# Kernel tuning notes

Measured on AMD Instinct MI355X. Metric: run time of the kernel, lower is better.

The kernel has to match this reference:

```python
import jax, jax.numpy as jnp
import numpy as np

B, S, D, H = 4, 2048, 768, 12
HD = D // H  # head_dim = 64
NEG = 1e10
EPS = 1e-5

def setup_inputs() -> dict:
    key = jax.random.key(0)
    k1, k2, k3 = jax.random.split(key, 3)
    return {
        "context": jax.random.normal(k1, (B, S, D), dtype=jnp.float32),
        "pad_mask": jnp.ones((B, S), dtype=jnp.float32),
        "w_qkv": jax.random.normal(k2, (D, 3 * D), dtype=jnp.float32) * 0.02,
        "w_proj": jax.random.normal(k3, (D, D), dtype=jnp.float32) * (0.02 / np.sqrt(2.0 * 12)),
        "b_proj": jnp.zeros((D,), dtype=jnp.float32),
        "gamma": jnp.ones((D,), dtype=jnp.float32),
        "beta": jnp.zeros((D,), dtype=jnp.float32),
    }

def reference(context, pad_mask, w_qkv, w_proj, b_proj, gamma, beta):
    b, s, d = context.shape
    resid = context
    qkv = context @ w_qkv                       # [B,S,3D]
    q, k, v = jnp.split(qkv, 3, axis=-1)
    # [B,S,D] -> [B,H,S,HD]
    q = q.reshape(b, s, H, HD).transpose(0, 2, 1, 3)
    k = k.reshape(b, s, H, HD).transpose(0, 2, 1, 3)
    v = v.reshape(b, s, H, HD).transpose(0, 2, 1, 3)
    scores = jnp.einsum("bhqd,bhkd->bhqk", q, k) * (1.0 / np.sqrt(HD))
    m = pad_mask[:, None, None, :]              # [B,1,1,S]
    scores = scores * m - (1.0 - m) * NEG       # multiplicative mask + big negative
    attn = jax.nn.softmax(scores, axis=-1)      # dropout is identity at inference
    out = jnp.einsum("bhqk,bhkd->bhqd", attn, v)
    out = out.transpose(0, 2, 1, 3).reshape(b, s, d)
    out = out @ w_proj + b_proj
    x = out + resid
    mu = jnp.mean(x, axis=-1, keepdims=True)
    var = jnp.var(x, axis=-1, keepdims=True)
    return (x - mu) * jax.lax.rsqrt(var + EPS) * gamma + beta
```

## Files before the change

kernel.cpp:

```cpp
#include <hip/hip_runtime.h>

#define BB 4
#define SS 2048
#define DD 768
#define HH 12
#define HDD 64
#define BS (BB*SS)
#define NQKV (3*DD)
#define NEL (BS*DD)

typedef __attribute__((ext_vector_type(8))) __bf16 bf16x8;
typedef __attribute__((ext_vector_type(4))) float fx4;
typedef __attribute__((ext_vector_type(4))) int   ix4;

#define MFMA16(a,b,c) __builtin_amdgcn_mfma_f32_16x16x32_bf16((a),(b),(c),0,0,0)

__device__ __forceinline__ unsigned short f2bf(float f) {
  unsigned u = __builtin_bit_cast(unsigned, f);
  u = (u + 0x7FFFu + ((u >> 16) & 1u)) >> 16;
  return (unsigned short)u;
}
__device__ __forceinline__ unsigned pkbf(float a, float b) {
  unsigned ua = __builtin_bit_cast(unsigned, a);
  unsigned ub = __builtin_bit_cast(unsigned, b);
  return ((ua + 0x8000u) >> 16) | ((ub + 0x8000u) & 0xFFFF0000u);
}

__global__ __launch_bounds__(256) void pack_bf16(const float* __restrict__ x,
                                                 unsigned short* __restrict__ y, int n4) {
  int i = blockIdx.x * 256 + threadIdx.x;
  if (i < n4) {
    float4 v = ((const float4*)x)[i];
    ((uint2*)y)[i] = make_uint2(pkbf(v.x, v.y), pkbf(v.z, v.w));
  }
}

__global__ __launch_bounds__(256) void pack_transpose(const float* __restrict__ w,
                                                      unsigned short* __restrict__ wT,
                                                      int K, int N) {
  __shared__ unsigned short t[32][33];
  int n0 = blockIdx.x * 32, k0 = blockIdx.y * 32;
  int tx = threadIdx.x & 31, ty = threadIdx.x >> 5;
#pragma unroll
  for (int r = ty; r < 32; r += 8)
    t[tx][r] = f2bf(w[(size_t)(k0 + r) * N + n0 + tx]);
  __syncthreads();
#pragma unroll
  for (int r = ty; r < 32; r += 8)
    wT[(size_t)(n0 + r) * K + k0 + tx] = t[r][tx];
}

__global__ __launch_bounds__(256) void gemm_qkv_k(const unsigned short* __restrict__ Wt,
                                                  const unsigned short* __restrict__ X,
                                                  unsigned short* __restrict__ Qo,
                                                  unsigned short* __restrict__ Ko,
                                                  unsigned short* __restrict__ Vto) {
  __shared__ unsigned short As[128 * 32];
  __shared__ unsigned short Bs[128 * 32];
  const int tid = threadIdx.x;
  const int w = tid >> 6, lane = tid & 63, quad = lane >> 4, l16 = lane & 15;
  const int m0 = blockIdx.y << 7;
  const int n0 = blockIdx.x << 7;
  const int wm = (w & 1) * 64, wn = (w >> 1) * 64;
  fx4 acc[4][4];
#pragma unroll
  for (int i = 0; i < 4; ++i)
#pragma unroll
    for (int c = 0; c < 4; ++c) acc[i][c] = (fx4){0.f, 0.f, 0.f, 0.f};

  const int c0 = tid, c1 = 256 + tid;
  const unsigned short* Ag0 = Wt + (size_t)(m0 + (c0 >> 2)) * DD + (c0 & 3) * 8;
  const unsigned short* Ag1 = Wt + (size_t)(m0 + (c1 >> 2)) * DD + (c1 & 3) * 8;
  const unsigned short* Bg0 = X + (size_t)(n0 + (c0 >> 2)) * DD + (c0 & 3) * 8;
  const unsigned short* Bg1 = X + (size_t)(n0 + (c1 >> 2)) * DD + (c1 & 3) * 8;

  ix4 ra0 = *(const ix4*)Ag0;
  ix4 ra1 = *(const ix4*)Ag1;
  ix4 rb0 = *(const ix4*)Bg0;
  ix4 rb1 = *(const ix4*)Bg1;

  for (int k0 = 0; k0 < DD; k0 += 32) {
    __syncthreads();
    *(ix4*)((char*)As + c0 * 16) = ra0;
    *(ix4*)((char*)As + c1 * 16) = ra1;
    *(ix4*)((char*)Bs + c0 * 16) = rb0;
    *(ix4*)((char*)Bs + c1 * 16) = rb1;
    __syncthreads();
    if (k0 + 32 < DD) {
      ra0 = *(const ix4*)(Ag0 + k0 + 32);
      ra1 = *(const ix4*)(Ag1 + k0 + 32);
      rb0 = *(const ix4*)(Bg0 + k0 + 32);
      rb1 = *(const ix4*)(Bg1 + k0 + 32);
    }
    bf16x8 af[4], bf[4];
#pragma unroll
    for (int i = 0; i < 4; ++i) af[i] = *(const bf16x8*)&As[(wm + i * 16 + l16) * 32 + quad * 8];
#pragma unroll
    for (int c = 0; c < 4; ++c) bf[c] = *(const bf16x8*)&Bs[(wn + c * 16 + l16) * 32 + quad * 8];
#pragma unroll
    for (int i = 0; i < 4; ++i)
#pragma unroll
      for (int c = 0; c < 4; ++c) acc[i][c] = MFMA16(af[i], bf[c], acc[i][c]);
  }

  const int which = m0 / DD;
#pragma unroll
  for (int i = 0; i < 4; ++i) {
    int fb = m0 + wm + i * 16 + quad * 4;
    int d = fb - which * DD;
    int h = d >> 6, hd = d & 63;
#pragma unroll
    for (int c = 0; c < 4; ++c) {
      int srow = n0 + wn + c * 16 + l16;
      int b = srow >> 11, s = srow & (SS - 1);
      if (which == 0) {
        uint2 v = make_uint2(pkbf(acc[i][c][0], acc[i][c][1]), pkbf(acc[i][c][2], acc[i][c][3]));
        *(uint2*)&Qo[((size_t)(b * HH + h) * SS + s) * HDD + hd] = v;
      } else if (which == 1) {
        uint2 v = make_uint2(pkbf(acc[i][c][0], acc[i][c][1]), pkbf(acc[i][c][2], acc[i][c][3]));
        *(uint2*)&Ko[((size_t)(b * HH + h) * SS + s) * HDD + hd] = v;
      } else {
#pragma unroll
        for (int r = 0; r < 4; ++r)
          Vto[((size_t)(b * HH + h) * HDD + hd + r) * SS + s] = f2bf(acc[i][c][r]);
      }
    }
  }
}

__global__ __launch_bounds__(256) void gemm_proj_k(const unsigned short* __restrict__ Wt,
                                                   const unsigned short* __restrict__ X,
                                                   const float* __restrict__ ctx,
                                                   const float* __restrict__ bproj,
                                                   float* __restrict__ xf) {
  __shared__ unsigned short As[128 * 32];
  __shared__ unsigned short Bs[128 * 32];
  const int tid = threadIdx.x;
  const int w = tid >> 6, lane = tid & 63, quad = lane >> 4, l16 = lane & 15;
  const int m0 = blockIdx.y << 7;
  const int n0 = blockIdx.x << 7;
  const int wm = (w & 1) * 64, wn = (w >> 1) * 64;
  fx4 acc[4][4];
#pragma unroll
  for (int i = 0; i < 4; ++i)
#pragma unroll
    for (int c = 0; c < 4; ++c) acc[i][c] = (fx4){0.f, 0.f, 0.f, 0.f};

  const int c0 = tid, c1 = 256 + tid;
  const unsigned short* Ag0 = Wt + (size_t)(m0 + (c0 >> 2)) * DD + (c0 & 3) * 8;
  const unsigned short* Ag1 = Wt + (size_t)(m0 + (c1 >> 2)) * DD + (c1 & 3) * 8;
  const unsigned short* Bg0 = X + (size_t)(n0 + (c0 >> 2)) * DD + (c0 & 3) * 8;
  const unsigned short* Bg1 = X + (size_t)(n0 + (c1 >> 2)) * DD + (c1 & 3) * 8;

  ix4 ra0 = *(const ix4*)Ag0;
  ix4 ra1 = *(const ix4*)Ag1;
  ix4 rb0 = *(const ix4*)Bg0;
  ix4 rb1 = *(const ix4*)Bg1;

  for (int k0 = 0; k0 < DD; k0 += 32) {
    __syncthreads();
    *(ix4*)((char*)As + c0 * 16) = ra0;
    *(ix4*)((char*)As + c1 * 16) = ra1;
    *(ix4*)((char*)Bs + c0 * 16) = rb0;
    *(ix4*)((char*)Bs + c1 * 16) = rb1;
    __syncthreads();
    if (k0 + 32 < DD) {
      ra0 = *(const ix4*)(Ag0 + k0 + 32);
      ra1 = *(const ix4*)(Ag1 + k0 + 32);
      rb0 = *(const ix4*)(Bg0 + k0 + 32);
      rb1 = *(const ix4*)(Bg1 + k0 + 32);
    }
    bf16x8 af[4], bf[4];
#pragma unroll
    for (int i = 0; i < 4; ++i) af[i] = *(const bf16x8*)&As[(wm + i * 16 + l16) * 32 + quad * 8];
#pragma unroll
    for (int c = 0; c < 4; ++c) bf[c] = *(const bf16x8*)&Bs[(wn + c * 16 + l16) * 32 + quad * 8];
#pragma unroll
    for (int i = 0; i < 4; ++i)
#pragma unroll
      for (int c = 0; c < 4; ++c) acc[i][c] = MFMA16(af[i], bf[c], acc[i][c]);
  }

#pragma unroll
  for (int i = 0; i < 4; ++i) {
    int fb = m0 + wm + i * 16 + quad * 4;
    float4 bp = *(const float4*)&bproj[fb];
#pragma unroll
    for (int c = 0; c < 4; ++c) {
      int srow = n0 + wn + c * 16 + l16;
      float4 cx = *(const float4*)&ctx[(size_t)srow * DD + fb];
      float4 r;
      r.x = acc[i][c][0] + bp.x + cx.x;
      r.y = acc[i][c][1] + bp.y + cx.y;
      r.z = acc[i][c][2] + bp.z + cx.z;
      r.w = acc[i][c][3] + bp.w + cx.w;
      *(float4*)&xf[(size_t)srow * DD + fb] = r;
    }
  }
}

__global__ __launch_bounds__(256) void attn_k(const unsigned short* __restrict__ Q,
                                              const unsigned short* __restrict__ K,
                                              const unsigned short* __restrict__ Vt,
                                              const float* __restrict__ mask,
                                              unsigned short* __restrict__ O) {
  __shared__ unsigned short Ks[64 * 64];
  __shared__ unsigned short Vts[64 * 64];
  const int tid = threadIdx.x;
  const int w = tid >> 6, lane = tid & 63;
  const int quad = lane >> 4, l16 = lane & 15;
  const int bh = blockIdx.y;
  const int b = bh / HH, h = bh - b * HH;
  const int q0 = blockIdx.x << 7;
  const unsigned short* Qb = Q + (size_t)bh * (SS * HDD);
  const unsigned short* Kb = K + (size_t)bh * (SS * HDD);
  const unsigned short* Vtb = Vt + (size_t)bh * (SS * HDD);
  const float* mb = mask + b * SS;

  bf16x8 qf[2][2];
#pragma unroll
  for (int qi = 0; qi < 2; ++qi)
#pragma unroll
    for (int f = 0; f < 2; ++f)
      qf[qi][f] = *(const bf16x8*)&Qb[(size_t)(q0 + w * 32 + qi * 16 + l16) * HDD + f * 32 + quad * 8];

  fx4 o[2][4];
#pragma unroll
  for (int qi = 0; qi < 2; ++qi)
#pragma unroll
    for (int ht = 0; ht < 4; ++ht) o[qi][ht] = (fx4){0.f, 0.f, 0.f, 0.f};
  float lsum[2] = {0.f, 0.f};

  const int cA = tid, cB = 256 + tid;
  const int rA = cA >> 3, pA = (cA & 7) ^ (rA & 7);
  const int rB = cB >> 3, pB = (cB & 7) ^ (rB & 7);

  ix4 rk0 = *(const ix4*)&Kb[(size_t)rA * HDD + pA * 8];
  ix4 rk1 = *(const ix4*)&Kb[(size_t)rB * HDD + pB * 8];
  ix4 rv0 = *(const ix4*)&Vtb[(size_t)rA * SS + pA * 8];
  ix4 rv1 = *(const ix4*)&Vtb[(size_t)rB * SS + pB * 8];

  for (int k0 = 0; k0 < SS; k0 += 64) {
    __syncthreads();
    *(ix4*)((char*)Ks + cA * 16) = rk0;
    *(ix4*)((char*)Ks + cB * 16) = rk1;
    *(ix4*)((char*)Vts + cA * 16) = rv0;
    *(ix4*)((char*)Vts + cB * 16) = rv1;
    __syncthreads();
    if (k0 + 64 < SS) {
      int kn = k0 + 64;
      rk0 = *(const ix4*)&Kb[(size_t)(kn + rA) * HDD + pA * 8];
      rk1 = *(const ix4*)&Kb[(size_t)(kn + rB) * HDD + pB * 8];
      rv0 = *(const ix4*)&Vtb[(size_t)rA * SS + kn + pA * 8];
      rv1 = *(const ix4*)&Vtb[(size_t)rB * SS + kn + pB * 8];
    }

    float4 mq[4];
#pragma unroll
    for (int kt = 0; kt < 4; ++kt)
      mq[kt] = *(const float4*)&mb[k0 + kt * 16 + quad * 4];

    bf16x8 kf[4][2];
#pragma unroll
    for (int kt = 0; kt < 4; ++kt) {
      int row = kt * 16 + l16;
      int rx = row & 7;
#pragma unroll
      for (int f = 0; f < 2; ++f)
        kf[kt][f] = *(const bf16x8*)&Ks[row * 64 + ((f * 4 + quad) ^ rx) * 8];
    }
    bf16x8 vf[4][2];
#pragma unroll
    for (int ht = 0; ht < 4; ++ht) {
      int row = ht * 16 + l16;
      int rx = row & 7;
#pragma unroll
      for (int f = 0; f < 2; ++f) {
        int dc0 = (f * 4 + (quad >> 1)) ^ rx;
        int dc1 = (f * 4 + 2 + (quad >> 1)) ^ rx;
        uint2 lo = *(const uint2*)((const char*)Vts + row * 128 + dc0 * 16 + (quad & 1) * 8);
        uint2 hi = *(const uint2*)((const char*)Vts + row * 128 + dc1 * 16 + (quad & 1) * 8);
        ix4 vv = (ix4){(int)lo.x, (int)lo.y, (int)hi.x, (int)hi.y};
        vf[ht][f] = __builtin_bit_cast(bf16x8, vv);
      }
    }

#pragma unroll
    for (int qi = 0; qi < 2; ++qi) {
      fx4 sc[4];
#pragma unroll
      for (int kt = 0; kt < 4; ++kt) {
        fx4 s = (fx4){0.f, 0.f, 0.f, 0.f};
        s = MFMA16(kf[kt][0], qf[qi][0], s);
        s = MFMA16(kf[kt][1], qf[qi][1], s);
        sc[kt] = s;
      }
      unsigned pk[4][2];
      float ls = 0.f;
#pragma unroll
      for (int kt = 0; kt < 4; ++kt) {
        float p[4];
#pragma unroll
        for (int r = 0; r < 4; ++r) {
          float mv = ((const float*)&mq[kt])[r];
          p[r] = __expf(sc[kt][r] * (0.125f * mv) - (1.f - mv) * 1e10f);
          ls += p[r];
        }
        pk[kt][0] = pkbf(p[0], p[1]);
        pk[kt][1] = pkbf(p[2], p[3]);
      }
      lsum[qi] += ls;
      ix4 p0 = (ix4){(int)pk[0][0], (int)pk[0][1], (int)pk[1][0], (int)pk[1][1]};
      ix4 p1 = (ix4){(int)pk[2][0], (int)pk[2][1], (int)pk[3][0], (int)pk[3][1]};
      bf16x8 pf0 = __builtin_bit_cast(bf16x8, p0);
      bf16x8 pf1 = __builtin_bit_cast(bf16x8, p1);
#pragma unroll
      for (int ht = 0; ht < 4; ++ht) {
        o[qi][ht] = MFMA16(vf[ht][0], pf0, o[qi][ht]);
        o[qi][ht] = MFMA16(vf[ht][1], pf1, o[qi][ht]);
      }
    }
  }

#pragma unroll
  for (int qi = 0; qi < 2; ++qi) {
    float t = lsum[qi];
    t += __shfl_xor(t, 16);
    t += __shfl_xor(t, 32);
    float inv = 1.f / fmaxf(t, 1e-30f);
    int sq = q0 + w * 32 + qi * 16 + l16;
    unsigned short* orow = O + ((size_t)(b * SS + sq)) * DD + h * HDD;
#pragma unroll
    for (int ht = 0; ht < 4; ++ht) {
      uint2 v = make_uint2(pkbf(o[qi][ht][0] * inv, o[qi][ht][1] * inv),
                           pkbf(o[qi][ht][2] * inv, o[qi][ht][3] * inv));
      *(uint2*)&orow[ht * 16 + quad * 4] = v;
    }
  }
}

__global__ __launch_bounds__(256) void ln_k(const float* __restrict__ x,
                                            const float* __restrict__ gamma,
                                            const float* __restrict__ beta,
                                            float* __restrict__ out) {
  const int row = blockIdx.x;
  const float* xr = x + (size_t)row * DD;
  const int t = threadIdx.x;
  float v0 = xr[t], v1 = xr[t + 256], v2 = xr[t + 512];
  float s = v0 + v1 + v2;
  float ss = v0 * v0 + v1 * v1 + v2 * v2;
#pragma unroll
  for (int d = 32; d > 0; d >>= 1) {
    s += __shfl_down(s, d);
    ss += __shfl_down(ss, d);
  }
  __shared__ float sh[10];
  int wv = t >> 6, lane = t & 63;
  if (lane == 0) { sh[wv] = s; sh[4 + wv] = ss; }
  __syncthreads();
  if (t == 0) {
    float S = sh[0] + sh[1] + sh[2] + sh[3];
    float SSm = sh[4] + sh[5] + sh[6] + sh[7];
    float mu = S * (1.0f / DD);
    float var = SSm * (1.0f / DD) - mu * mu;
    sh[8] = mu;
    sh[9] = rsqrtf(var + 1e-5f);
  }
  __syncthreads();
  float mu = sh[8], rstd = sh[9];
  out[(size_t)row * DD + t]       = (v0 - mu) * rstd * gamma[t]       + beta[t];
  out[(size_t)row * DD + t + 256] = (v1 - mu) * rstd * gamma[t + 256] + beta[t + 256];
  out[(size_t)row * DD + t + 512] = (v2 - mu) * rstd * gamma[t + 512] + beta[t + 512];
}

extern "C" void kernel_launch(void* const* d_in, const int* in_sizes, int n_in,
                              void* d_out, int out_size, void* d_ws, size_t ws_size,
                              hipStream_t stream) {
  (void)in_sizes; (void)n_in; (void)out_size; (void)ws_size;
  const float* ctx   = (const float*)d_in[0];
  const float* mask  = (const float*)d_in[1];
  const float* wqkv  = (const float*)d_in[2];
  const float* wproj = (const float*)d_in[3];
  const float* bproj = (const float*)d_in[4];
  const float* gamma = (const float*)d_in[5];
  const float* beta  = (const float*)d_in[6];
  float* out = (float*)d_out;

  char* p = (char*)d_ws;
  unsigned short* Xbf = (unsigned short*)p; p += (size_t)NEL * 2;
  unsigned short* Qw  = (unsigned short*)p; p += (size_t)NEL * 2;
  unsigned short* Kw  = (unsigned short*)p; p += (size_t)NEL * 2;
  unsigned short* Vtw = (unsigned short*)p; p += (size_t)NEL * 2;
  unsigned short* Ao  = (unsigned short*)p; p += (size_t)NEL * 2;
  unsigned short* WqkvT  = (unsigned short*)p; p += (size_t)DD * NQKV * 2;
  unsigned short* WprojT = (unsigned short*)p; p += (size_t)DD * DD * 2;
  float* xf = (float*)Qw;

  pack_bf16<<<NEL / 4 / 256, 256, 0, stream>>>(ctx, Xbf, NEL / 4);
  pack_transpose<<<dim3(NQKV / 32, DD / 32), 256, 0, stream>>>(wqkv, WqkvT, DD, NQKV);
  pack_transpose<<<dim3(DD / 32, DD / 32), 256, 0, stream>>>(wproj, WprojT, DD, DD);
  gemm_qkv_k<<<dim3(BS / 128, NQKV / 128), 256, 0, stream>>>(WqkvT, Xbf, Qw, Kw, Vtw);
  attn_k<<<dim3(SS / 128, BB * HH), 256, 0, stream>>>(Qw, Kw, Vtw, mask, Ao);
  gemm_proj_k<<<dim3(BS / 128, DD / 128), 256, 0, stream>>>(WprojT, Ao, ctx, bproj, xf);
  ln_k<<<BS, 256, 0, stream>>>(xf, gamma, beta, out);
}
```

Baseline: 276.5 us.

## Use direct global-to-LDS loads in GEMMs and streamline attention softmax

Both GEMM kernels drop register-staged prefetch and instead use global_load_lds to write tiles straight into shared memory, with a barrier before and after the compute. The attention kernel folds scale and mask into one FMA feeding exp2, packs probabilities with the hardware bf16 convert, and computes the row sums with an MFMA against a ones vector instead of scalar adds and shuffles. The GEMM change removes VGPR staging and LDS store instructions but loses the overlap of the next tile's load with the current MFMAs, since the load now completes before compute. The MFMA row sum adds matrix work but takes VALU adds off the softmax path. It also sums the bf16-rounded probabilities rather than the fp32 ones.

```diff
diff --git a/kernel.cpp b/kernel.cpp
--- a/kernel.cpp
+++ b/kernel.cpp
@@ -15,6 +15,10 @@
 
 #define MFMA16(a,b,c) __builtin_amdgcn_mfma_f32_16x16x32_bf16((a),(b),(c),0,0,0)
 
+#define GLLDS(g, l) __builtin_amdgcn_global_load_lds( \
+    (const __attribute__((address_space(1))) void*)(g), \
+    (__attribute__((address_space(3))) void*)(l), 16, 0, 0)
+
 __device__ __forceinline__ unsigned short f2bf(float f) {
   unsigned u = __builtin_bit_cast(unsigned, f);
   u = (u + 0x7FFFu + ((u >> 16) & 1u)) >> 16;
@@ -25,6 +29,12 @@
   unsigned ub = __builtin_bit_cast(unsigned, b);
   return ((ua + 0x8000u) >> 16) | ((ub + 0x8000u) & 0xFFFF0000u);
 }
+__device__ __forceinline__ unsigned cvtpk(float a, float b) {
+  unsigned r;
+  asm("v_cvt_pk_bf16_f32 %0, %1, %2" : "=v"(r) : "v"(a), "v"(b));
+  return r;
+}
+__device__ __forceinline__ float ex2(float x) { return __builtin_amdgcn_exp2f(x); }
 
 __global__ __launch_bounds__(256) void pack_bf16(const float* __restrict__ x,
                                                  unsigned short* __restrict__ y, int n4) {
@@ -73,25 +83,14 @@
   const unsigned short* Ag1 = Wt + (size_t)(m0 + (c1 >> 2)) * DD + (c1 & 3) * 8;
   const unsigned short* Bg0 = X + (size_t)(n0 + (c0 >> 2)) * DD + (c0 & 3) * 8;
   const unsigned short* Bg1 = X + (size_t)(n0 + (c1 >> 2)) * DD + (c1 & 3) * 8;
-
-  ix4 ra0 = *(const ix4*)Ag0;
-  ix4 ra1 = *(const ix4*)Ag1;
-  ix4 rb0 = *(const ix4*)Bg0;
-  ix4 rb1 = *(const ix4*)Bg1;
+  const int wb = w * 1024;
 
   for (int k0 = 0; k0 < DD; k0 += 32) {
-    __syncthreads();
-    *(ix4*)((char*)As + c0 * 16) = ra0;
-    *(ix4*)((char*)As + c1 * 16) = ra1;
-    *(ix4*)((char*)Bs + c0 * 16) = rb0;
-    *(ix4*)((char*)Bs + c1 * 16) = rb1;
-    __syncthreads();
-    if (k0 + 32 < DD) {
-      ra0 = *(const ix4*)(Ag0 + k0 + 32);
-      ra1 = *(const ix4*)(Ag1 + k0 + 32);
-      rb0 = *(const ix4*)(Bg0 + k0 + 32);
-      rb1 = *(const ix4*)(Bg1 + k0 + 32);
-    }
+    GLLDS(Ag0 + k0, (char*)As + wb);
+    GLLDS(Ag1 + k0, (char*)As + 4096 + wb);
+    GLLDS(Bg0 + k0, (char*)Bs + wb);
+    GLLDS(Bg1 + k0, (char*)Bs + 4096 + wb);
+    __syncthreads();
     bf16x8 af[4], bf[4];
 #pragma unroll
     for (int i = 0; i < 4; ++i) af[i] = *(const bf16x8*)&As[(wm + i * 16 + l16) * 32 + quad * 8];
@@ -101,6 +100,7 @@
     for (int i = 0; i < 4; ++i)
 #pragma unroll
       for (int c = 0; c < 4; ++c) acc[i][c] = MFMA16(af[i], bf[c], acc[i][c]);
+    __syncthreads();
   }
 
   const int which = m0 / DD;
@@ -151,25 +151,14 @@
   const unsigned short* Ag1 = Wt + (size_t)(m0 + (c1 >> 2)) * DD + (c1 & 3) * 8;
   const unsigned short* Bg0 = X + (size_t)(n0 + (c0 >> 2)) * DD + (c0 & 3) * 8;
   const unsigned short* Bg1 = X + (size_t)(n0 + (c1 >> 2)) * DD + (c1 & 3) * 8;
-
-  ix4 ra0 = *(const ix4*)Ag0;
-  ix4 ra1 = *(const ix4*)Ag1;
-  ix4 rb0 = *(const ix4*)Bg0;
-  ix4 rb1 = *(const ix4*)Bg1;
+  const int wb = w * 1024;
 
   for (int k0 = 0; k0 < DD; k0 += 32) {
-    __syncthreads();
-    *(ix4*)((char*)As + c0 * 16) = ra0;
-    *(ix4*)((char*)As + c1 * 16) = ra1;
-    *(ix4*)((char*)Bs + c0 * 16) = rb0;
-    *(ix4*)((char*)Bs + c1 * 16) = rb1;
-    __syncthreads();
-    if (k0 + 32 < DD) {
-      ra0 = *(const ix4*)(Ag0 + k0 + 32);
-      ra1 = *(const ix4*)(Ag1 + k0 + 32);
-      rb0 = *(const ix4*)(Bg0 + k0 + 32);
-      rb1 = *(const ix4*)(Bg1 + k0 + 32);
-    }
+    GLLDS(Ag0 + k0, (char*)As + wb);
+    GLLDS(Ag1 + k0, (char*)As + 4096 + wb);
+    GLLDS(Bg0 + k0, (char*)Bs + wb);
+    GLLDS(Bg1 + k0, (char*)Bs + 4096 + wb);
+    __syncthreads();
     bf16x8 af[4], bf[4];
 #pragma unroll
     for (int i = 0; i < 4; ++i) af[i] = *(const bf16x8*)&As[(wm + i * 16 + l16) * 32 + quad * 8];
@@ -179,6 +168,7 @@
     for (int i = 0; i < 4; ++i)
 #pragma unroll
       for (int c = 0; c < 4; ++c) acc[i][c] = MFMA16(af[i], bf[c], acc[i][c]);
+    __syncthreads();
   }
 
 #pragma unroll
@@ -229,7 +219,12 @@
   for (int qi = 0; qi < 2; ++qi)
 #pragma unroll
     for (int ht = 0; ht < 4; ++ht) o[qi][ht] = (fx4){0.f, 0.f, 0.f, 0.f};
-  float lsum[2] = {0.f, 0.f};
+  fx4 sacc[2];
+  sacc[0] = (fx4){0.f, 0.f, 0.f, 0.f};
+  sacc[1] = (fx4){0.f, 0.f, 0.f, 0.f};
+
+  const ix4 one4 = (ix4){0x3F803F80, 0x3F803F80, 0x3F803F80, 0x3F803F80};
+  const bf16x8 onesf = __builtin_bit_cast(bf16x8, one4);
 
   const int cA = tid, cB = 256 + tid;
   const int rA = cA >> 3, pA = (cA & 7) ^ (rA & 7);
@@ -255,10 +250,19 @@
       rv1 = *(const ix4*)&Vtb[(size_t)rB * SS + kn + pB * 8];
     }
 
-    float4 mq[4];
-#pragma unroll
-    for (int kt = 0; kt < 4; ++kt)
-      mq[kt] = *(const float4*)&mb[k0 + kt * 16 + quad * 4];
+    float4 mqa[4], mqb[4];
+#pragma unroll
+    for (int kt = 0; kt < 4; ++kt) {
+      float4 mq = *(const float4*)&mb[k0 + kt * 16 + quad * 4];
+      mqa[kt].x = mq.x * 0.18033688f;
+      mqa[kt].y = mq.y * 0.18033688f;
+      mqa[kt].z = mq.z * 0.18033688f;
+      mqa[kt].w = mq.w * 0.18033688f;
+      mqb[kt].x = __builtin_fmaf(mq.x, 1.44269504e10f, -1.44269504e10f);
+      mqb[kt].y = __builtin_fmaf(mq.y, 1.44269504e10f, -1.44269504e10f);
+      mqb[kt].z = __builtin_fmaf(mq.z, 1.44269504e10f, -1.44269504e10f);
+      mqb[kt].w = __builtin_fmaf(mq.w, 1.44269504e10f, -1.44269504e10f);
+    }
 
     bf16x8 kf[4][2];
 #pragma unroll
@@ -287,33 +291,27 @@
 
 #pragma unroll
     for (int qi = 0; qi < 2; ++qi) {
-      fx4 sc[4];
+      unsigned pw[8];
 #pragma unroll
       for (int kt = 0; kt < 4; ++kt) {
         fx4 s = (fx4){0.f, 0.f, 0.f, 0.f};
         s = MFMA16(kf[kt][0], qf[qi][0], s);
         s = MFMA16(kf[kt][1], qf[qi][1], s);
-        sc[kt] = s;
+        const float* ma = (const float*)&mqa[kt];
+        const float* mc = (const float*)&mqb[kt];
+        float p0 = ex2(__builtin_fmaf(s[0], ma[0], mc[0]));
+        float p1 = ex2(__builtin_fmaf(s[1], ma[1], mc[1]));
+        float p2 = ex2(__builtin_fmaf(s[2], ma[2], mc[2]));
+        float p3 = ex2(__builtin_fmaf(s[3], ma[3], mc[3]));
+        pw[kt * 2]     = cvtpk(p0, p1);
+        pw[kt * 2 + 1] = cvtpk(p2, p3);
       }
-      unsigned pk[4][2];
-      float ls = 0.f;
-#pragma unroll
-      for (int kt = 0; kt < 4; ++kt) {
-        float p[4];
-#pragma unroll
-        for (int r = 0; r < 4; ++r) {
-          float mv = ((const float*)&mq[kt])[r];
-          p[r] = __expf(sc[kt][r] * (0.125f * mv) - (1.f - mv) * 1e10f);
-          ls += p[r];
-        }
-        pk[kt][0] = pkbf(p[0], p[1]);
-        pk[kt][1] = pkbf(p[2], p[3]);
-      }
-      lsum[qi] += ls;
-      ix4 p0 = (ix4){(int)pk[0][0], (int)pk[0][1], (int)pk[1][0], (int)pk[1][1]};
-      ix4 p1 = (ix4){(int)pk[2][0], (int)pk[2][1], (int)pk[3][0], (int)pk[3][1]};
-      bf16x8 pf0 = __builtin_bit_cast(bf16x8, p0);
-      bf16x8 pf1 = __builtin_bit_cast(bf16x8, p1);
+      ix4 pi0 = (ix4){(int)pw[0], (int)pw[1], (int)pw[2], (int)pw[3]};
+      ix4 pi1 = (ix4){(int)pw[4], (int)pw[5], (int)pw[6], (int)pw[7]};
+      bf16x8 pf0 = __builtin_bit_cast(bf16x8, pi0);
+      bf16x8 pf1 = __builtin_bit_cast(bf16x8, pi1);
+      sacc[qi] = MFMA16(onesf, pf0, sacc[qi]);
+      sacc[qi] = MFMA16(onesf, pf1, sacc[qi]);
 #pragma unroll
       for (int ht = 0; ht < 4; ++ht) {
         o[qi][ht] = MFMA16(vf[ht][0], pf0, o[qi][ht]);
@@ -324,10 +322,7 @@
 
 #pragma unroll
   for (int qi = 0; qi < 2; ++qi) {
-    float t = lsum[qi];
-    t += __shfl_xor(t, 16);
-    t += __shfl_xor(t, 32);
-    float inv = 1.f / fmaxf(t, 1e-30f);
+    float inv = 1.f / fmaxf(sacc[qi][0], 1e-30f);
     int sq = q0 + w * 32 + qi * 16 + l16;
     unsigned short* orow = O + ((size_t)(b * SS + sq)) * DD + h * HDD;
 #pragma unroll
```

Result: faster. 258.6 us (-6.5%).
